# Kernel optimization log

Measured on AMD Instinct MI355X. Metric: run time of the kernel, lower is better.

The kernel has to match this reference:

```python
import jax, jax.numpy as jnp
import numpy as np

B, L, H, NH = 32, 512, 512, 8
HD = H // NH
SCALE = HD ** -0.5


def _heads(x):
    # (B, L, H) -> (B, NH, L, HD)
    return x.reshape(B, L, NH, HD).transpose(0, 2, 1, 3)


def _score(x, Wq, bq, Wk, bk):
    Q = _heads(x @ Wq.T + bq)
    K = _heads(x @ Wk.T + bk)
    return jnp.einsum('bhqd,bhkd->bhqk', Q, K) * SCALE


def setup_inputs() -> dict:
    key = jax.random.key(0)
    ks = jax.random.split(key, 16)
    d = {
        'seq_id': jax.random.normal(ks[0], (B, L, H), jnp.float32),
        'side_cate': jax.random.normal(ks[1], (B, L, H), jnp.float32),
        'side_brand': jax.random.normal(ks[2], (B, L, H), jnp.float32),
        'V_id_input': jax.random.normal(ks[3], (B, L, H), jnp.float32),
        'relative_time': jax.random.normal(ks[4], (B, NH, L, L), jnp.float32) * 0.02,
        'attn_mask': jnp.broadcast_to(jnp.tril(jnp.ones((L, L), bool)), (B, L, L)),
    }
    s = (2.0 / H) ** 0.5
    names = ['q_id', 'k_id', 'v', 'q_cate', 'k_cate', 'q_brand', 'k_brand', 'o']
    for i, n in enumerate(names):
        d['W' + n] = jax.random.normal(ks[5 + i], (H, H), jnp.float32) * s
        d['b' + n] = jnp.zeros((H,), jnp.float32)
    return d


def reference(seq_id, side_cate, side_brand, V_id_input, relative_time, attn_mask,
              Wq_id, bq_id, Wk_id, bk_id, Wv, bv,
              Wq_cate, bq_cate, Wk_cate, bk_cate,
              Wq_brand, bq_brand, Wk_brand, bk_brand,
              Wo, bo):
    V = _heads(V_id_input @ Wv.T + bv)  # (B, NH, L, HD)
    total = _score(seq_id, Wq_id, bq_id, Wk_id, bk_id)
    total = total + _score(side_cate, Wq_cate, bq_cate, Wk_cate, bk_cate)
    total = total + _score(side_brand, Wq_brand, bq_brand, Wk_brand, bk_brand)
    total = total + relative_time
    total = jnp.where(attn_mask[:, None], total, -jnp.inf)
    w = jax.nn.softmax(total.astype(jnp.float32), axis=-1).astype(total.dtype)
    w = jnp.nan_to_num(w, nan=0.0)
    # eval mode: dropout is identity
    attn_out = jnp.einsum('bhqk,bhkd->bhqd', w, V)
    attn_out = attn_out.transpose(0, 2, 1, 3).reshape(B, L, H)
    return attn_out @ Wo.T + bo
```

## Files before the change

kernel.cpp:

```cpp
#include <hip/hip_runtime.h>
#include <hip/hip_bf16.h>
#include <stdint.h>


typedef __bf16 bf16x8 __attribute__((ext_vector_type(8)));
typedef float f32x4 __attribute__((ext_vector_type(4)));

#define LOG2E 1.4426950408889634f

__device__ int g_isf32;
__device__ __align__(16) unsigned short g_Wbf[8 * 512 * 512];
__device__ __align__(16) unsigned short g_Xbv[32 * 512 * 512];

__device__ __forceinline__ f32x4 mfma16(bf16x8 a, bf16x8 b, f32x4 c) {
    return __builtin_amdgcn_mfma_f32_16x16x32_bf16(a, b, c, 0, 0, 0);
}

__device__ __forceinline__ float qmax16(float x) {
    x = fmaxf(x, __shfl_xor(x, 1));
    x = fmaxf(x, __shfl_xor(x, 2));
    x = fmaxf(x, __shfl_xor(x, 4));
    x = fmaxf(x, __shfl_xor(x, 8));
    return x;
}
__device__ __forceinline__ float qsum16(float x) {
    x += __shfl_xor(x, 1);
    x += __shfl_xor(x, 2);
    x += __shfl_xor(x, 4);
    x += __shfl_xor(x, 8);
    return x;
}

__device__ __forceinline__ float ldf(const void* p, size_t off, int isf) {
    return isf ? ((const float*)p)[off]
               : __bfloat162float(((const __hip_bfloat16*)p)[off]);
}

__device__ __forceinline__ void glds16(const void* g, void* l) {
    __builtin_amdgcn_global_load_lds(
        (const __attribute__((address_space(1))) void*)g,
        (__attribute__((address_space(3))) void*)l, 16, 0, 0);
}

__global__ void sniff_kernel(const unsigned short* __restrict__ p) {
    int t = threadIdx.x;
    int bad = 0, zc = 0;
    #pragma unroll
    for (int i = 0; i < 32; i++) {
        unsigned short u = p[(t * 32 + i) * 2];
        int e = (u >> 7) & 0xFF;
        bad |= (e >= 0xF0);
        zc += (u == 0);
    }
    unsigned long long mb = __ballot(bad != 0);
    #pragma unroll
    for (int s = 1; s < 64; s <<= 1) zc += __shfl_xor(zc, s);
    if (t == 0) g_isf32 = (mb != 0ull || zc > 1024) ? 1 : 0;
}

__global__ __launch_bounds__(256) void conv4(
    const float* __restrict__ s0, const float* __restrict__ s1,
    const float* __restrict__ s2, const float* __restrict__ s3,
    __hip_bfloat16* __restrict__ d0, __hip_bfloat16* __restrict__ d1,
    __hip_bfloat16* __restrict__ d2)
{
    if (!g_isf32) return;
    const int z = blockIdx.z;
    const float* s = (z == 0) ? s0 : (z == 1) ? s1 : (z == 2) ? s2 : s3;
    __hip_bfloat16* d = (z == 0) ? d0 : (z == 1) ? d1 : (z == 2) ? d2
                                      : (__hip_bfloat16*)g_Xbv;
    const int N8 = 32 * 512 * 512 / 8;
    for (int i = blockIdx.x * 256 + threadIdx.x; i < N8; i += gridDim.x * 256) {
        f32x4 a = ((const f32x4*)s)[2 * i];
        f32x4 b = ((const f32x4*)s)[2 * i + 1];
        bf16x8 o;
        o[0] = (__bf16)a[0]; o[1] = (__bf16)a[1]; o[2] = (__bf16)a[2]; o[3] = (__bf16)a[3];
        o[4] = (__bf16)b[0]; o[5] = (__bf16)b[1]; o[6] = (__bf16)b[2]; o[7] = (__bf16)b[3];
        ((bf16x8*)d)[i] = o;
    }
}

__global__ __launch_bounds__(256) void convW(
    const float* __restrict__ W0, const float* __restrict__ W1,
    const float* __restrict__ W2, const float* __restrict__ W3,
    const float* __restrict__ W4, const float* __restrict__ W5,
    const float* __restrict__ W6, const float* __restrict__ Wo)
{
    if (!g_isf32) return;
    const int z = blockIdx.z;
    const float* src;
    switch (z) {
        case 0: src = W0; break; case 1: src = W1; break;
        case 2: src = W2; break; case 3: src = W3; break;
        case 4: src = W4; break; case 5: src = W5; break;
        case 6: src = W6; break; default: src = Wo; break;
    }
    int i = blockIdx.x * 256 + threadIdx.x;
    f32x4 a = ((const f32x4*)src)[2 * i];
    f32x4 b = ((const f32x4*)src)[2 * i + 1];
    bf16x8 o;
    o[0] = (__bf16)a[0]; o[1] = (__bf16)a[1]; o[2] = (__bf16)a[2]; o[3] = (__bf16)a[3];
    o[4] = (__bf16)b[0]; o[5] = (__bf16)b[1]; o[6] = (__bf16)b[2]; o[7] = (__bf16)b[3];
    ((bf16x8*)g_Wbf)[z * 32768 + i] = o;
}

__global__ __launch_bounds__(256, 4) void gemm_all(
    const void* __restrict__ xs, const void* __restrict__ xc,
    const void* __restrict__ xb, const void* __restrict__ xv,
    const __hip_bfloat16* __restrict__ Xbs, const __hip_bfloat16* __restrict__ Xbc,
    const __hip_bfloat16* __restrict__ Xbb,
    const void* __restrict__ W0, const void* __restrict__ B0,
    const void* __restrict__ W1, const void* __restrict__ B1,
    const void* __restrict__ W2, const void* __restrict__ B2,
    const void* __restrict__ W3, const void* __restrict__ B3,
    const void* __restrict__ W4, const void* __restrict__ B4,
    const void* __restrict__ W5, const void* __restrict__ B5,
    const void* __restrict__ W6, const void* __restrict__ B6,
    const void* __restrict__ Wo, const void* __restrict__ Bo,
    const __hip_bfloat16* __restrict__ AO,
    __hip_bfloat16* __restrict__ Qcat, __hip_bfloat16* __restrict__ Kcat,
    __hip_bfloat16* __restrict__ Vt, void* __restrict__ Out,
    int oproj)
{
    __shared__ __align__(16) __hip_bfloat16 As[128 * 64];
    __shared__ __align__(16) __hip_bfloat16 Bs[128 * 64];

    const int isf = g_isf32;
    const int t = threadIdx.x;
    const int lane = t & 63, w = t >> 6;
    const int ln = lane & 15, hi = lane >> 4;
    const int wm = w >> 1, wn = w & 1;
    const int tm = blockIdx.x * 128, tn = blockIdx.y * 128;

    const __hip_bfloat16* Ab;
    const void *W, *bias;
    int kind = 3, comp = 0, wslot = 7;
    if (oproj) {
        Ab = AO; W = Wo; bias = Bo;
    } else {
        switch (blockIdx.z) {
            case 0:  Ab = isf ? Xbs : (const __hip_bfloat16*)xs;
                     W = W0; bias = B0; kind = 0; comp = 0; wslot = 0; break;
            case 1:  Ab = isf ? Xbs : (const __hip_bfloat16*)xs;
                     W = W1; bias = B1; kind = 1; comp = 0; wslot = 1; break;
            case 2:  Ab = isf ? (const __hip_bfloat16*)g_Xbv : (const __hip_bfloat16*)xv;
                     W = W2; bias = B2; kind = 2; comp = 0; wslot = 2; break;
            case 3:  Ab = isf ? Xbc : (const __hip_bfloat16*)xc;
                     W = W3; bias = B3; kind = 0; comp = 1; wslot = 3; break;
            case 4:  Ab = isf ? Xbc : (const __hip_bfloat16*)xc;
                     W = W4; bias = B4; kind = 1; comp = 1; wslot = 4; break;
            case 5:  Ab = isf ? Xbb : (const __hip_bfloat16*)xb;
                     W = W5; bias = B5; kind = 0; comp = 2; wslot = 5; break;
            default: Ab = isf ? Xbb : (const __hip_bfloat16*)xb;
                     W = W6; bias = B6; kind = 1; comp = 2; wslot = 6; break;
        }
    }
    const __hip_bfloat16* Wb = isf ? (const __hip_bfloat16*)g_Wbf + (size_t)wslot * 262144
                                   : (const __hip_bfloat16*)W;

    const int csw = (((lane & 7) ^ ((lane >> 3) & 7)) * 8);
    const int rsub = (w * 8) + (lane >> 3);

    f32x4 acc[4][4] = {};

    for (int k0 = 0; k0 < 512; k0 += 64) {
        #pragma unroll
        for (int r = 0; r < 4; r++)
            glds16(Ab + (size_t)(tm + r * 32 + rsub) * 512 + k0 + csw,
                   (char*)As + r * 4096 + w * 1024);
        #pragma unroll
        for (int r = 0; r < 4; r++)
            glds16(Wb + (size_t)(tn + r * 32 + rsub) * 512 + k0 + csw,
                   (char*)Bs + r * 4096 + w * 1024);
        __syncthreads();

        #pragma unroll
        for (int kk = 0; kk < 64; kk += 32) {
            bf16x8 af[4], bfr[4];
            #pragma unroll
            for (int i = 0; i < 4; i++)
                af[i] = *(const bf16x8*)&As[(wm * 64 + i * 16 + ln) * 64 +
                                            ((kk + hi * 8) ^ ((ln & 7) * 8))];
            #pragma unroll
            for (int j = 0; j < 4; j++)
                bfr[j] = *(const bf16x8*)&Bs[(wn * 64 + j * 16 + ln) * 64 +
                                             ((kk + hi * 8) ^ ((ln & 7) * 8))];
            #pragma unroll
            for (int i = 0; i < 4; i++)
                #pragma unroll
                for (int j = 0; j < 4; j++)
                    acc[i][j] = mfma16(af[i], bfr[j], acc[i][j]);
        }
        __syncthreads();
    }

    #pragma unroll
    for (int j = 0; j < 4; j++) {
        int col = tn + wn * 64 + j * 16 + ln;
        float bv = ldf(bias, col, isf);
        int h = col >> 6, d = col & 63;
        #pragma unroll
        for (int i = 0; i < 4; i++) {
            #pragma unroll
            for (int r = 0; r < 4; r++) {
                int row = tm + wm * 64 + i * 16 + hi * 4 + r;
                float val = acc[i][j][r] + bv;
                int b = row >> 9, l = row & 511;
                if (kind == 0)
                    Qcat[((size_t)(b * 8 + h) * 512 + l) * 192 + comp * 64 + d] =
                        __float2bfloat16(val);
                else if (kind == 1)
                    Kcat[((size_t)(b * 8 + h) * 512 + l) * 192 + comp * 64 + d] =
                        __float2bfloat16(val);
                else if (kind == 2)
                    Vt[((size_t)(b * 8 + h) * 64 + d) * 512 + l] =
                        __float2bfloat16(val);
                else if (isf)
                    ((float*)Out)[(size_t)row * 512 + col] = val;
                else
                    ((__hip_bfloat16*)Out)[(size_t)row * 512 + col] =
                        __float2bfloat16(val);
            }
        }
    }
}

__global__ __launch_bounds__(256, 2) void attn_kernel(
    const __hip_bfloat16* __restrict__ Qcat,
    const __hip_bfloat16* __restrict__ Kcat,
    const __hip_bfloat16* __restrict__ Vt,
    const void* __restrict__ rel,
    __hip_bfloat16* __restrict__ AO)
{
    __shared__ __align__(16) __hip_bfloat16 Ks[64 * 200];
    __shared__ __align__(16) __hip_bfloat16 Vs[64 * 72];
    __shared__ __align__(16) __hip_bfloat16 Ps[4 * 32 * 72];

    const int isf = g_isf32;
    const int t = threadIdx.x;
    const int lane = t & 63, w = t >> 6;
    const int ln = lane & 15, hi = lane >> 4;
    const int qt = blockIdx.x, h = blockIdx.y, b = blockIdx.z;
    const int qb = qt * 128;
    const size_t bh = (size_t)(b * 8 + h);

    const __hip_bfloat16* qc = Qcat + bh * 512 * 192;
    const __hip_bfloat16* kc = Kcat + bh * 512 * 192;
    const __hip_bfloat16* vp = Vt + bh * 64 * 512;
    const size_t rbase = bh * 512 * 512;

    bf16x8 qf[2][6];
    #pragma unroll
    for (int i = 0; i < 2; i++)
        #pragma unroll
        for (int kf = 0; kf < 6; kf++)
            qf[i][kf] = *(const bf16x8*)(qc + (size_t)(qb + w * 32 + i * 16 + ln) * 192
                                            + kf * 32 + hi * 8);

    float mst[2][4], lst[2][4];
    f32x4 oacc[2][4] = {};
    #pragma unroll
    for (int i = 0; i < 2; i++)
        #pragma unroll
        for (int r = 0; r < 4; r++) { mst[i][r] = -1e30f; lst[i][r] = 0.f; }

    const int nkt = 2 * qt + 2;
    for (int kt = 0; kt < nkt; kt++) {
        const int kb = kt * 64;
        __syncthreads();

        #pragma unroll
        for (int r = 0; r < 6; r++) {
            int e = r * 2048 + t * 8;
            int row = e / 192, col = e - row * 192;
            bf16x8 v = *(const bf16x8*)(kc + (size_t)(kb + row) * 192 + col);
            *(bf16x8*)&Ks[row * 200 + col] = v;
        }
        #pragma unroll
        for (int r = 0; r < 2; r++) {
            int e = r * 2048 + t * 8;
            int row = e >> 6, col = e & 63;
            bf16x8 v = *(const bf16x8*)(vp + (size_t)row * 512 + kb + col);
            *(bf16x8*)&Vs[row * 72 + col] = v;
        }
        __syncthreads();

        f32x4 s[2][4] = {};
        __builtin_amdgcn_s_setprio(1);
        #pragma unroll
        for (int kf = 0; kf < 6; kf++) {
            bf16x8 bfr[4];
            #pragma unroll
            for (int j = 0; j < 4; j++)
                bfr[j] = *(const bf16x8*)&Ks[(j * 16 + ln) * 200 + kf * 32 + hi * 8];
            #pragma unroll
            for (int i = 0; i < 2; i++)
                #pragma unroll
                for (int j = 0; j < 4; j++)
                    s[i][j] = mfma16(qf[i][kf], bfr[j], s[i][j]);
        }
        __builtin_amdgcn_s_setprio(0);

        #pragma unroll
        for (int i = 0; i < 2; i++) {
            #pragma unroll
            for (int r = 0; r < 4; r++) {
                int qrow = qb + w * 32 + i * 16 + hi * 4 + r;
                size_t roff = rbase + (size_t)qrow * 512 + kb;
                #pragma unroll
                for (int j = 0; j < 4; j++) {
                    int col = kb + j * 16 + ln;
                    float rv = ldf(rel, roff + j * 16 + ln, isf);
                    float v = fmaf(s[i][j][r], 0.125f * LOG2E, rv * LOG2E);
                    s[i][j][r] = (col > qrow) ? -1e30f : v;
                }
            }
        }

        #pragma unroll
        for (int i = 0; i < 2; i++) {
            #pragma unroll
            for (int r = 0; r < 4; r++) {
                float mx = fmaxf(fmaxf(s[i][0][r], s[i][1][r]),
                                 fmaxf(s[i][2][r], s[i][3][r]));
                mx = qmax16(mx);
                float mnew = fmaxf(mst[i][r], mx);
                float al = exp2f(mst[i][r] - mnew);
                float sum = 0.f;
                #pragma unroll
                for (int j = 0; j < 4; j++) {
                    float p = exp2f(s[i][j][r] - mnew);
                    s[i][j][r] = p;
                    sum += p;
                }
                sum = qsum16(sum);
                lst[i][r] = lst[i][r] * al + sum;
                mst[i][r] = mnew;
                #pragma unroll
                for (int jn = 0; jn < 4; jn++)
                    oacc[i][jn][r] *= al;
            }
        }

        __hip_bfloat16* pw = &Ps[w * 32 * 72];
        #pragma unroll
        for (int i = 0; i < 2; i++) {
            #pragma unroll
            for (int r = 0; r < 4; r++) {
                int prow = i * 16 + hi * 4 + r;
                #pragma unroll
                for (int j = 0; j < 4; j++)
                    pw[prow * 72 + j * 16 + ln] = __float2bfloat16(s[i][j][r]);
            }
        }
        __syncthreads();

        __builtin_amdgcn_s_setprio(1);
        #pragma unroll
        for (int kk = 0; kk < 64; kk += 32) {
            bf16x8 ap[2], bv[4];
            #pragma unroll
            for (int i = 0; i < 2; i++)
                ap[i] = *(const bf16x8*)&Ps[w * 2304 + (i * 16 + ln) * 72 + kk + hi * 8];
            #pragma unroll
            for (int jn = 0; jn < 4; jn++)
                bv[jn] = *(const bf16x8*)&Vs[(jn * 16 + ln) * 72 + kk + hi * 8];
            #pragma unroll
            for (int i = 0; i < 2; i++)
                #pragma unroll
                for (int jn = 0; jn < 4; jn++)
                    oacc[i][jn] = mfma16(ap[i], bv[jn], oacc[i][jn]);
        }
        __builtin_amdgcn_s_setprio(0);
    }

    #pragma unroll
    for (int i = 0; i < 2; i++) {
        #pragma unroll
        for (int r = 0; r < 4; r++) {
            int qrow = qb + w * 32 + i * 16 + hi * 4 + r;
            float inv = 1.0f / lst[i][r];
            __hip_bfloat16* orow = AO + ((size_t)(b * 512 + qrow)) * 512 + h * 64;
            #pragma unroll
            for (int jn = 0; jn < 4; jn++)
                orow[jn * 16 + ln] = __float2bfloat16(oacc[i][jn][r] * inv);
        }
    }
}

extern "C" void kernel_launch(void* const* d_in, const int* in_sizes, int n_in,
                              void* d_out, int out_size, void* d_ws, size_t ws_size,
                              hipStream_t stream) {
    (void)in_sizes; (void)n_in; (void)out_size; (void)ws_size;
    const void* xs  = d_in[0];
    const void* xc  = d_in[1];
    const void* xb  = d_in[2];
    const void* xv  = d_in[3];
    const void* rel = d_in[4];
    const void* W0 = d_in[6];    const void* B0 = d_in[7];
    const void* W1 = d_in[8];    const void* B1 = d_in[9];
    const void* W2 = d_in[10];   const void* B2 = d_in[11];
    const void* W3 = d_in[12];   const void* B3 = d_in[13];
    const void* W4 = d_in[14];   const void* B4 = d_in[15];
    const void* W5 = d_in[16];   const void* B5 = d_in[17];
    const void* W6 = d_in[18];   const void* B6 = d_in[19];
    const void* Wo = d_in[20];   const void* Bo = d_in[21];

    char* ws = (char*)d_ws;
    __hip_bfloat16* Qcat = (__hip_bfloat16*)(ws);
    __hip_bfloat16* Kcat = (__hip_bfloat16*)(ws + 50331648);
    __hip_bfloat16* Vt   = (__hip_bfloat16*)(ws + 100663296);
    __hip_bfloat16* AO   = (__hip_bfloat16*)(ws + 117440512);

    __hip_bfloat16* Xbs = AO;
    __hip_bfloat16* Xbc = (__hip_bfloat16*)d_out;
    __hip_bfloat16* Xbb = (__hip_bfloat16*)((char*)d_out + 16777216);

    dim3 blk(256, 1, 1);
    sniff_kernel<<<1, 64, 0, stream>>>((const unsigned short*)xs);
    conv4<<<dim3(1024, 1, 4), blk, 0, stream>>>(
        (const float*)xs, (const float*)xc, (const float*)xb, (const float*)xv,
        Xbs, Xbc, Xbb);
    convW<<<dim3(128, 1, 8), blk, 0, stream>>>(
        (const float*)W0, (const float*)W1, (const float*)W2, (const float*)W3,
        (const float*)W4, (const float*)W5, (const float*)W6, (const float*)Wo);
    gemm_all<<<dim3(128, 4, 7), blk, 0, stream>>>(
        xs, xc, xb, xv, Xbs, Xbc, Xbb,
        W0, B0, W1, B1, W2, B2, W3, B3, W4, B4, W5, B5, W6, B6,
        Wo, Bo, AO, Qcat, Kcat, Vt, d_out, 0);
    attn_kernel<<<dim3(4, 8, 32), blk, 0, stream>>>(Qcat, Kcat, Vt, rel, AO);
    gemm_all<<<dim3(128, 4, 1), blk, 0, stream>>>(
        xs, xc, xb, xv, Xbs, Xbc, Xbb,
        W0, B0, W1, B1, W2, B2, W3, B3, W4, B4, W5, B5, W6, B6,
        Wo, Bo, AO, Qcat, Kcat, Vt, d_out, 1);
}
```

Before: 679.9 us.

## Merge conversion kernels, vectorize GEMM epilogue stores, prefetch K/V tiles in attention

Folds the weight conversion into the activation conversion kernel, which saves one launch. The GEMM epilogue now stages each output tile through shared memory so Q/K/output rows are written as 16-byte vectors, and V-transpose rows as 8-byte vectors, instead of scattered 2-byte stores. The attention kernel loads the next K/V tile into registers while the current tile is being computed, hiding global-load latency. In exchange it uses more registers, and the GEMM launch-bounds occupancy hint drops from 4 to 3.

```diff
diff --git a/kernel.cpp b/kernel.cpp
--- a/kernel.cpp
+++ b/kernel.cpp
@@ -4,6 +4,7 @@
 
 
 typedef __bf16 bf16x8 __attribute__((ext_vector_type(8)));
+typedef __bf16 bf16x4 __attribute__((ext_vector_type(4)));
 typedef float f32x4 __attribute__((ext_vector_type(4)));
 
 #define LOG2E 1.4426950408889634f
@@ -58,14 +59,36 @@
     if (t == 0) g_isf32 = (mb != 0ull || zc > 1024) ? 1 : 0;
 }
 
-__global__ __launch_bounds__(256) void conv4(
+__global__ __launch_bounds__(256) void conv_all(
     const float* __restrict__ s0, const float* __restrict__ s1,
     const float* __restrict__ s2, const float* __restrict__ s3,
+    const float* __restrict__ W0, const float* __restrict__ W1,
+    const float* __restrict__ W2, const float* __restrict__ W3,
+    const float* __restrict__ W4, const float* __restrict__ W5,
+    const float* __restrict__ W6, const float* __restrict__ W7,
     __hip_bfloat16* __restrict__ d0, __hip_bfloat16* __restrict__ d1,
     __hip_bfloat16* __restrict__ d2)
 {
     if (!g_isf32) return;
     const int z = blockIdx.z;
+    if (z == 4) {
+        const int wi = blockIdx.x >> 7;
+        const float* src;
+        switch (wi) {
+            case 0: src = W0; break; case 1: src = W1; break;
+            case 2: src = W2; break; case 3: src = W3; break;
+            case 4: src = W4; break; case 5: src = W5; break;
+            case 6: src = W6; break; default: src = W7; break;
+        }
+        int i = (blockIdx.x & 127) * 256 + threadIdx.x;
+        f32x4 a = ((const f32x4*)src)[2 * i];
+        f32x4 b = ((const f32x4*)src)[2 * i + 1];
+        bf16x8 o;
+        o[0] = (__bf16)a[0]; o[1] = (__bf16)a[1]; o[2] = (__bf16)a[2]; o[3] = (__bf16)a[3];
+        o[4] = (__bf16)b[0]; o[5] = (__bf16)b[1]; o[6] = (__bf16)b[2]; o[7] = (__bf16)b[3];
+        ((bf16x8*)g_Wbf)[wi * 32768 + i] = o;
+        return;
+    }
     const float* s = (z == 0) ? s0 : (z == 1) ? s1 : (z == 2) ? s2 : s3;
     __hip_bfloat16* d = (z == 0) ? d0 : (z == 1) ? d1 : (z == 2) ? d2
                                       : (__hip_bfloat16*)g_Xbv;
@@ -80,31 +103,7 @@
     }
 }
 
-__global__ __launch_bounds__(256) void convW(
-    const float* __restrict__ W0, const float* __restrict__ W1,
-    const float* __restrict__ W2, const float* __restrict__ W3,
-    const float* __restrict__ W4, const float* __restrict__ W5,
-    const float* __restrict__ W6, const float* __restrict__ Wo)
-{
-    if (!g_isf32) return;
-    const int z = blockIdx.z;
-    const float* src;
-    switch (z) {
-        case 0: src = W0; break; case 1: src = W1; break;
-        case 2: src = W2; break; case 3: src = W3; break;
-        case 4: src = W4; break; case 5: src = W5; break;
-        case 6: src = W6; break; default: src = Wo; break;
-    }
-    int i = blockIdx.x * 256 + threadIdx.x;
-    f32x4 a = ((const f32x4*)src)[2 * i];
-    f32x4 b = ((const f32x4*)src)[2 * i + 1];
-    bf16x8 o;
-    o[0] = (__bf16)a[0]; o[1] = (__bf16)a[1]; o[2] = (__bf16)a[2]; o[3] = (__bf16)a[3];
-    o[4] = (__bf16)b[0]; o[5] = (__bf16)b[1]; o[6] = (__bf16)b[2]; o[7] = (__bf16)b[3];
-    ((bf16x8*)g_Wbf)[z * 32768 + i] = o;
-}
-
-__global__ __launch_bounds__(256, 4) void gemm_all(
+__global__ __launch_bounds__(256, 3) void gemm_all(
     const void* __restrict__ xs, const void* __restrict__ xc,
     const void* __restrict__ xb, const void* __restrict__ xv,
     const __hip_bfloat16* __restrict__ Xbs, const __hip_bfloat16* __restrict__ Xbc,
@@ -122,8 +121,9 @@
     __hip_bfloat16* __restrict__ Vt, void* __restrict__ Out,
     int oproj)
 {
-    __shared__ __align__(16) __hip_bfloat16 As[128 * 64];
-    __shared__ __align__(16) __hip_bfloat16 Bs[128 * 64];
+    __shared__ __align__(16) char smem[32768];
+    __hip_bfloat16* As = (__hip_bfloat16*)smem;
+    __hip_bfloat16* Bs = (__hip_bfloat16*)(smem + 16384);
 
     const int isf = g_isf32;
     const int t = threadIdx.x;
@@ -167,11 +167,11 @@
         #pragma unroll
         for (int r = 0; r < 4; r++)
             glds16(Ab + (size_t)(tm + r * 32 + rsub) * 512 + k0 + csw,
-                   (char*)As + r * 4096 + w * 1024);
+                   smem + r * 4096 + w * 1024);
         #pragma unroll
         for (int r = 0; r < 4; r++)
             glds16(Wb + (size_t)(tn + r * 32 + rsub) * 512 + k0 + csw,
-                   (char*)Bs + r * 4096 + w * 1024);
+                   smem + 16384 + r * 4096 + w * 1024);
         __syncthreads();
 
         #pragma unroll
@@ -194,32 +194,64 @@
         __syncthreads();
     }
 
-    #pragma unroll
-    for (int j = 0; j < 4; j++) {
-        int col = tn + wn * 64 + j * 16 + ln;
-        float bv = ldf(bias, col, isf);
-        int h = col >> 6, d = col & 63;
-        #pragma unroll
-        for (int i = 0; i < 4; i++) {
-            #pragma unroll
-            for (int r = 0; r < 4; r++) {
-                int row = tm + wm * 64 + i * 16 + hi * 4 + r;
-                float val = acc[i][j][r] + bv;
-                int b = row >> 9, l = row & 511;
-                if (kind == 0)
-                    Qcat[((size_t)(b * 8 + h) * 512 + l) * 192 + comp * 64 + d] =
-                        __float2bfloat16(val);
-                else if (kind == 1)
-                    Kcat[((size_t)(b * 8 + h) * 512 + l) * 192 + comp * 64 + d] =
-                        __float2bfloat16(val);
-                else if (kind == 2)
-                    Vt[((size_t)(b * 8 + h) * 64 + d) * 512 + l] =
-                        __float2bfloat16(val);
-                else if (isf)
-                    ((float*)Out)[(size_t)row * 512 + col] = val;
-                else
-                    ((__hip_bfloat16*)Out)[(size_t)row * 512 + col] =
-                        __float2bfloat16(val);
+    if (kind == 2) {
+        #pragma unroll
+        for (int j = 0; j < 4; j++) {
+            int col = tn + wn * 64 + j * 16 + ln;
+            float bv = ldf(bias, col, isf);
+            int h = col >> 6, d = col & 63;
+            #pragma unroll
+            for (int i = 0; i < 4; i++) {
+                int row0 = tm + wm * 64 + i * 16 + hi * 4;
+                int b = row0 >> 9, l0 = row0 & 511;
+                bf16x4 pv;
+                #pragma unroll
+                for (int r = 0; r < 4; r++)
+                    pv[r] = (__bf16)(acc[i][j][r] + bv);
+                *(bf16x4*)&Vt[((size_t)(b * 8 + h) * 64 + d) * 512 + l0] = pv;
+            }
+        }
+    } else {
+        float* Tw = (float*)(smem + w * 5120);
+        #pragma unroll
+        for (int j = 0; j < 4; j++) {
+            int cb = tn + wn * 64 + j * 16;
+            float bv = ldf(bias, cb + ln, isf);
+            #pragma unroll
+            for (int i = 0; i < 4; i++)
+                #pragma unroll
+                for (int r = 0; r < 4; r++)
+                    Tw[(i * 16 + hi * 4 + r) * 20 + ln] = acc[i][j][r] + bv;
+            int mg = tm + wm * 64 + lane;
+            f32x4 t0 = *(const f32x4*)&Tw[lane * 20 + 0];
+            f32x4 t1 = *(const f32x4*)&Tw[lane * 20 + 4];
+            f32x4 t2 = *(const f32x4*)&Tw[lane * 20 + 8];
+            f32x4 t3 = *(const f32x4*)&Tw[lane * 20 + 12];
+            if (kind == 3 && isf) {
+                float* op = (float*)Out + (size_t)mg * 512 + cb;
+                *(f32x4*)(op + 0) = t0;  *(f32x4*)(op + 4) = t1;
+                *(f32x4*)(op + 8) = t2;  *(f32x4*)(op + 12) = t3;
+            } else {
+                bf16x8 o0, o1;
+                o0[0] = (__bf16)t0[0]; o0[1] = (__bf16)t0[1];
+                o0[2] = (__bf16)t0[2]; o0[3] = (__bf16)t0[3];
+                o0[4] = (__bf16)t1[0]; o0[5] = (__bf16)t1[1];
+                o0[6] = (__bf16)t1[2]; o0[7] = (__bf16)t1[3];
+                o1[0] = (__bf16)t2[0]; o1[1] = (__bf16)t2[1];
+                o1[2] = (__bf16)t2[2]; o1[3] = (__bf16)t2[3];
+                o1[4] = (__bf16)t3[0]; o1[5] = (__bf16)t3[1];
+                o1[6] = (__bf16)t3[2]; o1[7] = (__bf16)t3[3];
+                __hip_bfloat16* dp;
+                if (kind == 3) {
+                    dp = (__hip_bfloat16*)Out + (size_t)mg * 512 + cb;
+                } else {
+                    int b = mg >> 9, l = mg & 511;
+                    int h = cb >> 6, d0 = cb & 63;
+                    dp = (kind == 0 ? Qcat : Kcat) +
+                         ((size_t)(b * 8 + h) * 512 + l) * 192 + comp * 64 + d0;
+                }
+                *(bf16x8*)dp = o0;
+                *(bf16x8*)(dp + 8) = o1;
             }
         }
     }
@@ -257,6 +289,13 @@
             qf[i][kf] = *(const bf16x8*)(qc + (size_t)(qb + w * 32 + i * 16 + ln) * 192
                                             + kf * 32 + hi * 8);
 
+    int krow[6], kcol[6];
+    #pragma unroll
+    for (int r = 0; r < 6; r++) {
+        int e = r * 2048 + t * 8;
+        krow[r] = e / 192; kcol[r] = e - krow[r] * 192;
+    }
+
     float mst[2][4], lst[2][4];
     f32x4 oacc[2][4] = {};
     #pragma unroll
@@ -265,25 +304,42 @@
         for (int r = 0; r < 4; r++) { mst[i][r] = -1e30f; lst[i][r] = 0.f; }
 
     const int nkt = 2 * qt + 2;
+
+    bf16x8 kreg[6], vreg[2];
+    #pragma unroll
+    for (int r = 0; r < 6; r++)
+        kreg[r] = *(const bf16x8*)(kc + (size_t)krow[r] * 192 + kcol[r]);
+    #pragma unroll
+    for (int r = 0; r < 2; r++) {
+        int e = r * 2048 + t * 8;
+        vreg[r] = *(const bf16x8*)(vp + (size_t)(e >> 6) * 512 + (e & 63));
+    }
+
     for (int kt = 0; kt < nkt; kt++) {
         const int kb = kt * 64;
         __syncthreads();
 
         #pragma unroll
-        for (int r = 0; r < 6; r++) {
-            int e = r * 2048 + t * 8;
-            int row = e / 192, col = e - row * 192;
-            bf16x8 v = *(const bf16x8*)(kc + (size_t)(kb + row) * 192 + col);
-            *(bf16x8*)&Ks[row * 200 + col] = v;
-        }
+        for (int r = 0; r < 6; r++)
+            *(bf16x8*)&Ks[krow[r] * 200 + kcol[r]] = kreg[r];
         #pragma unroll
         for (int r = 0; r < 2; r++) {
             int e = r * 2048 + t * 8;
-            int row = e >> 6, col = e & 63;
-            bf16x8 v = *(const bf16x8*)(vp + (size_t)row * 512 + kb + col);
-            *(bf16x8*)&Vs[row * 72 + col] = v;
+            *(bf16x8*)&Vs[(e >> 6) * 72 + (e & 63)] = vreg[r];
         }
         __syncthreads();
+
+        if (kt + 1 < nkt) {
+            const int kb2 = kb + 64;
+            #pragma unroll
+            for (int r = 0; r < 6; r++)
+                kreg[r] = *(const bf16x8*)(kc + (size_t)(kb2 + krow[r]) * 192 + kcol[r]);
+            #pragma unroll
+            for (int r = 0; r < 2; r++) {
+                int e = r * 2048 + t * 8;
+                vreg[r] = *(const bf16x8*)(vp + (size_t)(e >> 6) * 512 + kb2 + (e & 63));
+            }
+        }
 
         f32x4 s[2][4] = {};
         __builtin_amdgcn_s_setprio(1);
@@ -418,12 +474,11 @@
 
     dim3 blk(256, 1, 1);
     sniff_kernel<<<1, 64, 0, stream>>>((const unsigned short*)xs);
-    conv4<<<dim3(1024, 1, 4), blk, 0, stream>>>(
+    conv_all<<<dim3(1024, 1, 5), blk, 0, stream>>>(
         (const float*)xs, (const float*)xc, (const float*)xb, (const float*)xv,
+        (const float*)W0, (const float*)W1, (const float*)W2, (const float*)W3,
+        (const float*)W4, (const float*)W5, (const float*)W6, (const float*)Wo,
         Xbs, Xbc, Xbb);
-    convW<<<dim3(128, 1, 8), blk, 0, stream>>>(
-        (const float*)W0, (const float*)W1, (const float*)W2, (const float*)W3,
-        (const float*)W4, (const float*)W5, (const float*)W6, (const float*)Wo);
     gemm_all<<<dim3(128, 4, 7), blk, 0, stream>>>(
         xs, xc, xb, xv, Xbs, Xbc, Xbb,
         W0, B0, W1, B1, W2, B2, W3, B3, W4, B4, W5, B5, W6, B6,
```

Result: slower. 724.1 us (+6.5%).
